# Optimization experiments

Hardware: AMD Instinct MI355X
Metric: run time of the kernel (lower is better)

The kernel has to match this reference:

```python
import jax, jax.numpy as jnp
import numpy as np

HID = 2048
H = 16
D_NOPE = 128
D_ROPE = 64
HEAD_DIM = D_NOPE + D_ROPE  # 192
V_DIM = 128
KV_RANK = 512
Q_RANK = 1536
THETA = 10000.0
EPS = 1e-6
B, S = 2, 2048


def _rope_cos_sin(seq_len):
    # half-dim frequencies: cos/sin have shape (seq_len, D_ROPE//2)
    inv_freq = 1.0 / (THETA ** (jnp.arange(0, D_ROPE, 2, dtype=jnp.float32) / D_ROPE))
    freqs = jnp.arange(seq_len, dtype=jnp.float32)[:, None] * inv_freq[None, :]
    return jnp.cos(freqs), jnp.sin(freqs)


def _apply_rope(x, cos, sin):
    # x: (..., D_ROPE); cos/sin broadcastable to (..., D_ROPE//2)
    half = x.shape[-1] // 2
    x1, x2 = x[..., :half], x[..., half:]
    return jnp.concatenate([x1 * cos - x2 * sin, x2 * cos + x1 * sin], axis=-1)


def _rmsnorm(x, w):
    ms = jnp.mean(jnp.square(x), axis=-1, keepdims=True)
    return x * jax.lax.rsqrt(ms + EPS) * w


def setup_inputs() -> dict:
    key = jax.random.key(0)
    ks = jax.random.split(key, 7)
    std = 0.02
    return {
        "x": jax.random.normal(ks[0], (B, S, HID), dtype=jnp.float32),
        "w_q_down": jax.random.normal(ks[1], (HID, Q_RANK), dtype=jnp.float32) * std,
        "w_q_up": jax.random.normal(ks[2], (Q_RANK, H * HEAD_DIM), dtype=jnp.float32) * std,
        "w_kv_down": jax.random.normal(ks[3], (HID, KV_RANK + D_ROPE), dtype=jnp.float32) * std,
        "kv_norm_w": jnp.ones((KV_RANK,), dtype=jnp.float32),
        "w_kv_up": jax.random.normal(ks[4], (KV_RANK, H * (D_NOPE + V_DIM)), dtype=jnp.float32) * std,
        "w_out": jax.random.normal(ks[5], (H * V_DIM, HID), dtype=jnp.float32) * std,
    }


def reference(x, w_q_down, w_q_up, w_kv_down, kv_norm_w, w_kv_up, w_out):
    b, s, _ = x.shape
    scale = 1.0 / np.sqrt(HEAD_DIM)

    # query: low-rank down then up, split into nope/rope parts
    q = (x @ w_q_down) @ w_q_up                      # (b, s, H*HEAD_DIM)
    q = q.reshape(b, s, H, HEAD_DIM)
    q_nope, q_rope = q[..., :D_NOPE], q[..., D_NOPE:]

    # KV: compressed latent + rope key component
    kv_full = x @ w_kv_down                          # (b, s, KV_RANK + D_ROPE)
    kv_c, k_rope = kv_full[..., :KV_RANK], kv_full[..., KV_RANK:]
    kv_c = _rmsnorm(kv_c, kv_norm_w)

    kv_exp = (kv_c @ w_kv_up).reshape(b, s, H, D_NOPE + V_DIM)
    k_nope, v = kv_exp[..., :D_NOPE], kv_exp[..., D_NOPE:]

    # RoPE (no past_kv -> q_offset = 0, kv_len = s)
    cos, sin = _rope_cos_sin(s)                      # (s, D_ROPE//2)
    cos4, sin4 = cos[None, :, None, :], sin[None, :, None, :]
    q_rope = _apply_rope(q_rope, cos4, sin4)         # (b, s, H, D_ROPE)
    k_rope = _apply_rope(k_rope, cos[None], sin[None])  # (b, s, D_ROPE)

    k_rope_h = jnp.broadcast_to(k_rope[:, :, None, :], (b, s, H, D_ROPE))
    k = jnp.concatenate([k_nope, k_rope_h], axis=-1)     # (b, s, H, HEAD_DIM)
    q_full = jnp.concatenate([q_nope, q_rope], axis=-1)  # (b, s, H, HEAD_DIM)

    # causal SDPA
    scores = jnp.einsum("bqhd,bkhd->bhqk", q_full, k) * scale
    causal = jnp.tril(jnp.ones((s, s), dtype=bool))
    scores = jnp.where(causal[None, None], scores, jnp.finfo(scores.dtype).min)
    attn = jax.nn.softmax(scores, axis=-1)
    out = jnp.einsum("bhqk,bkhd->bqhd", attn, v)     # (b, s, H, V_DIM)
    out = out.reshape(b, s, H * V_DIM)
    return out @ w_out
```

## Files before the change

kernel.cpp:

```cpp
#include <hip/hip_runtime.h>
#include <hip/hip_bf16.h>
#include <math.h>

#define HID    2048
#define NH     16
#define D_NOPE 128
#define D_ROPE 64
#define HD     192
#define V_DIM  128
#define KV_RANK 512
#define Q_RANK  1536
#define BATCH  2
#define SEQ    2048
#define ROWS   (BATCH*SEQ)

typedef __attribute__((ext_vector_type(8))) short short8;
typedef __attribute__((ext_vector_type(4))) float f32x4;

__device__ __forceinline__ unsigned short f2bf(float x) {
    unsigned int u = __float_as_uint(x);
    unsigned int r = (u + 0x7fffu + ((u >> 16) & 1u)) >> 16;
    return (unsigned short)r;
}
__device__ __forceinline__ float bf2f(unsigned short u) {
    return __uint_as_float((unsigned int)u << 16);
}

typedef const __attribute__((address_space(1))) unsigned int gu32;
typedef __attribute__((address_space(3))) unsigned int lu32;
__device__ __forceinline__ void gl_lds16(const void* g, void* l) {
    __builtin_amdgcn_global_load_lds((gu32*)g, (lu32*)l, 16, 0, 0);
}

template<int CTRL>
__device__ __forceinline__ float dpp_mv(float x) {
    return __int_as_float(__builtin_amdgcn_update_dpp(
        __float_as_int(x), __float_as_int(x), CTRL, 0xF, 0xF, true));
}
__device__ __forceinline__ float rowmax16(float x) {
    x = fmaxf(x, dpp_mv<0xB1>(x));
    x = fmaxf(x, dpp_mv<0x4E>(x));
    x = fmaxf(x, dpp_mv<0x141>(x));
    x = fmaxf(x, dpp_mv<0x140>(x));
    return x;
}

__global__ __launch_bounds__(256) void preprocess_kernel(
    const float* __restrict__ x,
    const float* __restrict__ w_q_down, const float* __restrict__ w_q_up,
    const float* __restrict__ w_kv_down, const float* __restrict__ w_kv_up,
    const float* __restrict__ w_out,
    float* __restrict__ table, unsigned short* __restrict__ xb,
    unsigned short* __restrict__ wt1, unsigned short* __restrict__ wt2,
    unsigned short* __restrict__ wt3, unsigned short* __restrict__ wt4,
    unsigned short* __restrict__ wt5)
{
    const int tid = threadIdx.x;
    int bid = blockIdx.x;

    if (bid < 512) {
        int idx = bid * 256 + tid;
        int pos = idx >> 6, u = idx & 63;
        int i = u & 31;
        float invf = expf((float)i * (-9.210340371976184f / 32.0f));
        float ang = (float)pos * invf;
        table[idx] = (u < 32) ? cosf(ang) : sinf(ang);
        return;
    }
    bid -= 512;
    if (bid < 8192) {
        size_t i = (size_t)(bid * 256 + tid) * 4;
        float4 v = *(const float4*)(x + i);
        ushort4 u;
        u.x = f2bf(v.x); u.y = f2bf(v.y); u.z = f2bf(v.z); u.w = f2bf(v.w);
        *(ushort4*)(xb + i) = u;
        return;
    }
    bid -= 8192;

    const float* src; unsigned short* dst; int K, N, gx, lb;
    if (bid < 768)       { src = w_q_down;  dst = wt1; K = 2048; N = 1536; gx = 24; lb = bid; }
    else if (bid < 1920) { src = w_q_up;    dst = wt2; K = 1536; N = 3072; gx = 48; lb = bid - 768; }
    else if (bid < 2208) { src = w_kv_down; dst = wt3; K = 2048; N = 576;  gx = 9;  lb = bid - 1920; }
    else if (bid < 2720) { src = w_kv_up;   dst = wt4; K = 512;  N = 4096; gx = 64; lb = bid - 2208; }
    else                 { src = w_out;     dst = wt5; K = 2048; N = 2048; gx = 32; lb = bid - 2720; }
    const int n0 = (lb % gx) * 64, k0 = (lb / gx) * 64;

    __shared__ float T[64][65];
    const int c4 = tid & 15, r = tid >> 4;
    #pragma unroll
    for (int i = 0; i < 4; i++) {
        int row = r + i * 16;
        float4 v = *(const float4*)(src + (size_t)(k0 + row) * N + n0 + c4 * 4);
        T[row][c4*4+0] = v.x; T[row][c4*4+1] = v.y;
        T[row][c4*4+2] = v.z; T[row][c4*4+3] = v.w;
    }
    __syncthreads();
    #pragma unroll
    for (int i = 0; i < 4; i++) {
        int nrow = r + i * 16;
        ushort4 u;
        u.x = f2bf(T[c4*4+0][nrow]); u.y = f2bf(T[c4*4+1][nrow]);
        u.z = f2bf(T[c4*4+2][nrow]); u.w = f2bf(T[c4*4+3][nrow]);
        *(ushort4*)(dst + (size_t)(n0 + nrow) * K + k0 + c4 * 4) = u;
    }
}

extern __shared__ unsigned short smem_gemm[];

template<int BN, bool OUT_BF16>
__device__ __forceinline__ void bgemm_body(
    int rbid, int nb,
    const unsigned short* __restrict__ A,
    const unsigned short* __restrict__ Bt,
    void* __restrict__ Cv,
    int M, int N, int K)
{
    constexpr int NT = BN / 32;
    constexpr int NSLAB = 8 + BN / 16;
    const int tid  = threadIdx.x;
    const int w    = tid >> 6;
    const int lane = tid & 63;
    const int n16  = lane & 15, quad = lane >> 4;

    const int T8   = nb >> 3;
    const int nbid = (rbid & 7) * T8 + (rbid >> 3);
    const int gx   = N / BN;
    const int m0 = (nbid / gx) * 128;
    const int n0 = (nbid % gx) * BN;
    const int moff = (w & 1) * 64;
    const int noff = (w >> 1) * (NT * 16);

    unsigned short* As = smem_gemm;
    unsigned short* Bs = smem_gemm + 128*32;

    const unsigned short* gp[4];
    unsigned short* lp[4];
    int ns = 0;
    const int rl = lane >> 2, sc = lane & 3;
    for (int s = w; s < NSLAB; s += 4) {
        int kc = sc ^ (((s * 16 + rl) >> 1) & 3);
        if (s < 8) {
            gp[ns] = A + (size_t)(m0 + s * 16 + rl) * K + kc * 8;
            lp[ns] = As + s * 512;
        } else {
            int sb = s - 8;
            gp[ns] = Bt + (size_t)(n0 + sb * 16 + rl) * K + kc * 8;
            lp[ns] = Bs + sb * 512;
        }
        ns++;
    }

    const int swz = (quad ^ ((n16 >> 1) & 3)) * 8;
    int aoff[4], boff[NT];
    #pragma unroll
    for (int mt = 0; mt < 4; mt++) aoff[mt] = (moff + mt * 16 + n16) * 32 + swz;
    #pragma unroll
    for (int nt = 0; nt < NT; nt++) boff[nt] = (noff + nt * 16 + n16) * 32 + swz;

    f32x4 acc[4][NT];
    #pragma unroll
    for (int mt = 0; mt < 4; mt++)
        #pragma unroll
        for (int nt = 0; nt < NT; nt++) acc[mt][nt] = (f32x4){0.f, 0.f, 0.f, 0.f};

    for (int k0 = 0; k0 < K; k0 += 32) {
        #pragma unroll
        for (int j = 0; j < 4; j++) if (j < ns) gl_lds16(gp[j], lp[j]);
        #pragma unroll
        for (int j = 0; j < 4; j++) if (j < ns) gp[j] += 32;
        __syncthreads();

        short8 af[4], bfr[NT];
        #pragma unroll
        for (int mt = 0; mt < 4; mt++) af[mt] = *(const short8*)(As + aoff[mt]);
        #pragma unroll
        for (int nt = 0; nt < NT; nt++) bfr[nt] = *(const short8*)(Bs + boff[nt]);
        #pragma unroll
        for (int mt = 0; mt < 4; mt++)
            #pragma unroll
            for (int nt = 0; nt < NT; nt++)
                acc[mt][nt] = __builtin_amdgcn_mfma_f32_16x16x32_bf16(
                    af[mt], bfr[nt], acc[mt][nt], 0, 0, 0);
        __syncthreads();
    }

    #pragma unroll
    for (int mt = 0; mt < 4; mt++)
        #pragma unroll
        for (int nt = 0; nt < NT; nt++)
            #pragma unroll
            for (int r = 0; r < 4; r++) {
                size_t idx = (size_t)(m0 + moff + mt * 16 + quad * 4 + r) * N
                           + n0 + noff + nt * 16 + n16;
                if (OUT_BF16) ((unsigned short*)Cv)[idx] = f2bf(acc[mt][nt][r]);
                else          ((float*)Cv)[idx] = acc[mt][nt][r];
            }
}

__global__ __launch_bounds__(256) void gemm_stage1_kernel(
    const unsigned short* __restrict__ xb,
    const unsigned short* __restrict__ wt1, const unsigned short* __restrict__ wt3,
    unsigned short* __restrict__ qdb, float* __restrict__ kv_full)
{
    if (blockIdx.x < 384)
        bgemm_body<128, true>(blockIdx.x, 384, xb, wt1, qdb, ROWS, 1536, 2048);
    else
        bgemm_body<64, false>(blockIdx.x - 384, 288, xb, wt3, kv_full, ROWS, 576, 2048);
}

__global__ __launch_bounds__(256) void gemm_stage2_kernel(
    const unsigned short* __restrict__ qdb, const unsigned short* __restrict__ wt2,
    const unsigned short* __restrict__ kv_cb, const unsigned short* __restrict__ wt4,
    unsigned short* __restrict__ qb16, unsigned short* __restrict__ kv_exp_b)
{
    if (blockIdx.x < 768)
        bgemm_body<128, true>(blockIdx.x, 768, qdb, wt2, qb16, ROWS, 3072, 1536);
    else
        bgemm_body<128, true>(blockIdx.x - 768, 1024, kv_cb, wt4, kv_exp_b, ROWS, 4096, 512);
}

__global__ __launch_bounds__(256) void gemm_out_kernel(
    const unsigned short* __restrict__ attnb, const unsigned short* __restrict__ wt5,
    float* __restrict__ out)
{
    bgemm_body<128, false>(blockIdx.x, 512, attnb, wt5, out, ROWS, 2048, 2048);
}

__global__ __launch_bounds__(256) void kv_norm_rope_kernel(
    const float* __restrict__ kv_full,
    const float* __restrict__ w,
    const float* __restrict__ table,
    unsigned short* __restrict__ kv_cb,
    unsigned short* __restrict__ k_rope_b)
{
    const int row = blockIdx.x;
    const int tid = threadIdx.x;
    const float* src = kv_full + (size_t)row * 576;
    float v0 = src[tid], v1 = src[tid + 256];
    float ss = v0*v0 + v1*v1;
    #pragma unroll
    for (int off = 32; off > 0; off >>= 1) ss += __shfl_down(ss, off);
    __shared__ float red[4];
    __shared__ float msh;
    if ((tid & 63) == 0) red[tid >> 6] = ss;
    __syncthreads();
    if (tid == 0) msh = (red[0] + red[1] + red[2] + red[3]) * (1.0f / 512.0f);
    __syncthreads();
    float f = rsqrtf(msh + 1e-6f);
    kv_cb[(size_t)row * 512 + tid]       = f2bf(v0 * f * w[tid]);
    kv_cb[(size_t)row * 512 + tid + 256] = f2bf(v1 * f * w[tid + 256]);
    if (tid < 32) {
        int pos = row & (SEQ - 1);
        float c = table[pos*64 + tid], s = table[pos*64 + 32 + tid];
        float x1 = src[512 + tid], x2 = src[512 + 32 + tid];
        k_rope_b[(size_t)row * 64 + tid]      = f2bf(x1*c - x2*s);
        k_rope_b[(size_t)row * 64 + 32 + tid] = f2bf(x2*c + x1*s);
    }
}

__global__ __launch_bounds__(256) void pack_vt_kernel(
    const unsigned short* __restrict__ kv_exp_b, unsigned short* __restrict__ Vmat)
{
    const int st = blockIdx.x;
    const int h  = blockIdx.y;
    const int b  = blockIdx.z;
    const int tid = threadIdx.x;
    const int s0 = st * 64;
    __shared__ float T[64][129];

    #pragma unroll
    for (int t = 0; t < 8; t++) {
        int idx = tid + t * 256;
        int tokr = idx >> 5, c4 = idx & 31;
        ushort4 u = *(const ushort4*)(kv_exp_b +
            ((size_t)(b*SEQ) + s0 + tokr) * 4096 + h*256 + 128 + c4*4);
        T[tokr][c4*4+0] = bf2f(u.x); T[tokr][c4*4+1] = bf2f(u.y);
        T[tokr][c4*4+2] = bf2f(u.z); T[tokr][c4*4+3] = bf2f(u.w);
    }
    __syncthreads();

    int d = tid >> 1, sh = (tid & 1) * 32;
    unsigned short* op = Vmat + ((size_t)((b*NH + h) * V_DIM + d)) * SEQ + s0 + sh;
    #pragma unroll
    for (int j = 0; j < 32; j += 2) {
        ushort2 u;
        u.x = f2bf(T[sh + j][d]);
        u.y = f2bf(T[sh + j + 1][d]);
        *(ushort2*)(op + j) = u;
    }
}

__global__ __launch_bounds__(256, 3) void flash_mfma_kernel(
    const unsigned short* __restrict__ qb16,
    const unsigned short* __restrict__ kv_exp_b,
    const unsigned short* __restrict__ k_rope_b,
    const unsigned short* __restrict__ Vmat,
    const float* __restrict__ table,
    unsigned short* __restrict__ attnb)
{
    const int bid  = blockIdx.x;
    const int xcd  = bid & 7, slot = bid >> 3;
    const int grp  = xcd + 8 * (slot >> 5);
    const int qb   = 31 - (slot & 31);
    const int h    = grp & 15, b = grp >> 4;
    const int tid  = threadIdx.x;
    const int w    = tid >> 6;
    const int lane = tid & 63;
    const int n16  = lane & 15;
    const int quad = lane >> 4;

    const int q0 = qb * 64 + w * 16;
    const char* kNopeB = (const char*)(kv_exp_b + (size_t)b * SEQ * 4096 + h * 256);
    const char* kRopeB = (const char*)(k_rope_b + (size_t)b * SEQ * 64);
    const char* vByte  = (const char*)(Vmat + (size_t)(b*NH + h) * V_DIM * SEQ);

    __shared__ unsigned short Ks[2][6144];
    __shared__ unsigned short Vs[2][4096];
    __shared__ unsigned short Plds[4][16][40];

    const char* gK[2]; int lK[2];
    #pragma unroll
    for (int t = 0; t < 2; t++) {
        int idx = t * 256 + tid;
        int kc = idx >> 7, key = (idx >> 2) & 31, sc = idx & 3;
        int scs = sc ^ ((key >> 1) & 3);
        gK[t] = kNopeB + (size_t)key * 8192 + kc * 64 + scs * 16;
        lK[t] = idx * 16;
    }
    const char* gR; int lR;
    {
        int kc = tid >> 7, key = (tid >> 2) & 31, sc = tid & 3;
        int scs = sc ^ ((key >> 1) & 3);
        gR = kRopeB + (size_t)key * 128 + kc * 64 + scs * 16;
        lR = (512 + tid) * 16;
    }
    const char* gV[2]; int lV[2];
    #pragma unroll
    for (int t = 0; t < 2; t++) {
        int idx = t * 256 + tid;
        int d = idx >> 2, sc = idx & 3;
        int scs = sc ^ ((d >> 1) & 3);
        gV[t] = vByte + (size_t)d * (SEQ * 2) + scs * 16;
        lV[t] = idx * 16;
    }

    auto stage = [&](int kt, int bufsel) {
        const size_t koff = (size_t)kt * 32;
        #pragma unroll
        for (int t = 0; t < 2; t++)
            gl_lds16(gK[t] + koff * 8192, (char*)Ks[bufsel] + lK[t]);
        gl_lds16(gR + koff * 128, (char*)Ks[bufsel] + lR);
        #pragma unroll
        for (int t = 0; t < 2; t++)
            gl_lds16(gV[t] + koff * 2, (char*)Vs[bufsel] + lV[t]);
    };

    short8 qf[6];
    {
        const unsigned short* qp = qb16 + ((size_t)(b*SEQ) + q0 + n16) * (NH*HD)
                                 + h * HD + quad * 8;
        #pragma unroll
        for (int kc = 0; kc < 6; kc++)
            qf[kc] = *(const short8*)(qp + kc * 32);
        const float* tb = table + (size_t)(q0 + n16) * 64 + quad * 8;
        float4 c0 = *(const float4*)(tb);
        float4 c1 = *(const float4*)(tb + 4);
        float4 s0 = *(const float4*)(tb + 32);
        float4 s1 = *(const float4*)(tb + 36);
        float cs[8] = {c0.x,c0.y,c0.z,c0.w,c1.x,c1.y,c1.z,c1.w};
        float sn[8] = {s0.x,s0.y,s0.z,s0.w,s1.x,s1.y,s1.z,s1.w};
        #pragma unroll
        for (int j = 0; j < 8; j++) {
            float x1 = bf2f((unsigned short)qf[4][j]);
            float x2 = bf2f((unsigned short)qf[5][j]);
            qf[4][j] = (short)f2bf(x1*cs[j] - x2*sn[j]);
            qf[5][j] = (short)f2bf(x2*cs[j] + x1*sn[j]);
        }
    }

    short8 onesf;
    #pragma unroll
    for (int j = 0; j < 8; j++) onesf[j] = (short)0x3F80;

    f32x4 O[9];
    #pragma unroll
    for (int c = 0; c < 9; c++) O[c] = (f32x4){0.f, 0.f, 0.f, 0.f};
    float mrow[4] = {-INFINITY, -INFINITY, -INFINITY, -INFINITY};

    const float SCLOG2 = 0.10412779736150104f;
    const float THRRAW = 83.14f;
    const int swz = (quad ^ ((n16 >> 1) & 3)) * 8;
    const int ntB = 2 * qb + 2;

    stage(0, 0);
    int cur = 0;
    for (int kt = 0; kt < ntB; kt++) {
        __syncthreads();
        if (kt + 1 < ntB) stage(kt + 1, cur ^ 1);
        const int k0 = kt * 32;

        if (k0 <= q0 + 15) {
            const unsigned short* KsB = Ks[cur];
            const unsigned short* VsB = Vs[cur];

            f32x4 S[2];
            __builtin_amdgcn_s_setprio(1);
            #pragma unroll
            for (int half = 0; half < 2; half++) {
                f32x4 acc = (f32x4){0.f, 0.f, 0.f, 0.f};
                const int keyoff = (half * 16 + n16) * 32 + swz;
                #pragma unroll
                for (int kc = 0; kc < 6; kc++) {
                    short8 kf = *(const short8*)(KsB + kc * 1024 + keyoff);
                    acc = __builtin_amdgcn_mfma_f32_16x16x32_bf16(qf[kc], kf, acc, 0, 0, 0);
                }
                S[half] = acc;
            }
            __builtin_amdgcn_s_setprio(0);

            float p0[4], p1[4];
            if (k0 + 32 > q0) {
                #pragma unroll
                for (int r = 0; r < 4; r++) {
                    int row = q0 + quad*4 + r;
                    p0[r] = (k0 + n16      <= row) ? S[0][r] : -INFINITY;
                    p1[r] = (k0 + 16 + n16 <= row) ? S[1][r] : -INFINITY;
                }
            } else {
                #pragma unroll
                for (int r = 0; r < 4; r++) { p0[r] = S[0][r]; p1[r] = S[1][r]; }
            }

            float tmax[4];
            float growth = -INFINITY;
            #pragma unroll
            for (int r = 0; r < 4; r++) {
                tmax[r] = rowmax16(fmaxf(p0[r], p1[r]));
                growth = fmaxf(growth, tmax[r] - mrow[r]);
            }
            if (!__all(growth <= THRRAW)) {
                #pragma unroll
                for (int r = 0; r < 4; r++) {
                    float mnew = fmaxf(mrow[r], tmax[r]);
                    float alpha = exp2f((mrow[r] - mnew) * SCLOG2);
                    mrow[r] = mnew;
                    #pragma unroll
                    for (int c = 0; c < 9; c++) O[c][r] *= alpha;
                }
            }
            #pragma unroll
            for (int r = 0; r < 4; r++) {
                float e0 = exp2f((p0[r] - mrow[r]) * SCLOG2);
                float e1 = exp2f((p1[r] - mrow[r]) * SCLOG2);
                unsigned int pk;
                asm("v_cvt_pk_bf16_f32 %0, %1, %2" : "=v"(pk) : "v"(e0), "v"(e1));
                unsigned short* pw = &Plds[w][quad*4 + r][0];
                pw[n16]      = (unsigned short)(pk & 0xffffu);
                pw[16 + n16] = (unsigned short)(pk >> 16);
            }

            short8 pf = *(const short8*)(&Plds[w][n16][quad * 8]);
            __builtin_amdgcn_s_setprio(1);
            #pragma unroll
            for (int c = 0; c < 8; c++) {
                short8 vf = *(const short8*)(VsB + (c * 16 + n16) * 32 + swz);
                O[c] = __builtin_amdgcn_mfma_f32_16x16x32_bf16(pf, vf, O[c], 0, 0, 0);
            }
            O[8] = __builtin_amdgcn_mfma_f32_16x16x32_bf16(pf, onesf, O[8], 0, 0, 0);
            __builtin_amdgcn_s_setprio(0);
        }
        cur ^= 1;
    }

    float invl[4];
    #pragma unroll
    for (int r = 0; r < 4; r++) invl[r] = 1.0f / O[8][r];
    #pragma unroll
    for (int c = 0; c < 8; c++) {
        #pragma unroll
        for (int r = 0; r < 4; r++) {
            size_t tok = (size_t)b * SEQ + q0 + quad*4 + r;
            attnb[tok * (NH*V_DIM) + h * V_DIM + c*16 + n16] = f2bf(O[c][r] * invl[r]);
        }
    }
}

extern "C" void kernel_launch(void* const* d_in, const int* in_sizes, int n_in,
                              void* d_out, int out_size, void* d_ws, size_t ws_size,
                              hipStream_t stream)
{
    const float* x         = (const float*)d_in[0];
    const float* w_q_down  = (const float*)d_in[1];
    const float* w_q_up    = (const float*)d_in[2];
    const float* w_kv_down = (const float*)d_in[3];
    const float* kv_norm_w = (const float*)d_in[4];
    const float* w_kv_up   = (const float*)d_in[5];
    const float* w_out     = (const float*)d_in[6];
    float* out = (float*)d_out;
    float* ws  = (float*)d_ws;

    float*          table    = ws;
    unsigned short* xb       = (unsigned short*)(ws + 131072);
    unsigned short* qdb      = (unsigned short*)(ws + 4325376);
    unsigned short* qb16     = (unsigned short*)(ws + 7471104);
    float*          kv_full  = ws + 13762560;
    unsigned short* kv_cb    = (unsigned short*)(ws + 16121856);
    unsigned short* k_rope_b = (unsigned short*)(ws + 17170432);
    unsigned short* kv_exp_b = (unsigned short*)(ws + 17301504);
    unsigned short* Vmat     = (unsigned short*)(ws + 25690112);
    unsigned short* attnb    = (unsigned short*)(ws + 29884416);
    unsigned short* wt1      = (unsigned short*)(ws + 34078720);
    unsigned short* wt2      = (unsigned short*)(ws + 35651584);
    unsigned short* wt3      = (unsigned short*)(ws + 38010880);
    unsigned short* wt4      = (unsigned short*)(ws + 38600704);
    unsigned short* wt5      = (unsigned short*)(ws + 39649280);

    preprocess_kernel<<<dim3(12448), 256, 0, stream>>>(
        x, w_q_down, w_q_up, w_kv_down, w_kv_up, w_out,
        table, xb, wt1, wt2, wt3, wt4, wt5);

    gemm_stage1_kernel<<<dim3(672), 256, 16384, stream>>>(xb, wt1, wt3, qdb, kv_full);

    kv_norm_rope_kernel<<<ROWS, 256, 0, stream>>>(kv_full, kv_norm_w, table, kv_cb, k_rope_b);

    gemm_stage2_kernel<<<dim3(1792), 256, 16384, stream>>>(qdb, wt2, kv_cb, wt4, qb16, kv_exp_b);

    pack_vt_kernel<<<dim3(SEQ/64, NH, BATCH), 256, 0, stream>>>(kv_exp_b, Vmat);

    flash_mfma_kernel<<<dim3(1024), 256, 0, stream>>>(qb16, kv_exp_b, k_rope_b, Vmat, table, attnb);

    gemm_out_kernel<<<dim3(512), 256, 16384, stream>>>(attnb, wt5, out);
}
```

Before: 431.3 us.

## Fuse V transpose into kv-up GEMM epilogue and shrink GEMM M-tiles

The kv-up GEMM epilogue now writes V tiles straight into the transposed Vmat layout with 4-token vector stores, so the separate pack_vt kernel and its extra read of kv_exp_b go away. The GEMM template also gains a BM parameter, and stage1 and the output GEMM switch to 64-row tiles with twice the blocks, aimed at better CU occupancy and load balance. Smaller tiles mean less reuse of each B tile. The transposed epilogue stores are strided by SEQ, which may coalesce worse.

```diff
diff --git a/kernel.cpp b/kernel.cpp
--- a/kernel.cpp
+++ b/kernel.cpp
@@ -108,16 +108,18 @@
 
 extern __shared__ unsigned short smem_gemm[];
 
-template<int BN, bool OUT_BF16>
+template<int BM, int BN, bool OUT_BF16, bool VSTORE>
 __device__ __forceinline__ void bgemm_body(
     int rbid, int nb,
     const unsigned short* __restrict__ A,
     const unsigned short* __restrict__ Bt,
     void* __restrict__ Cv,
+    unsigned short* __restrict__ vmat,
     int M, int N, int K)
 {
+    constexpr int MT = BM / 32;
     constexpr int NT = BN / 32;
-    constexpr int NSLAB = 8 + BN / 16;
+    constexpr int NSLAB = BM / 16 + BN / 16;
     const int tid  = threadIdx.x;
     const int w    = tid >> 6;
     const int lane = tid & 63;
@@ -126,13 +128,13 @@
     const int T8   = nb >> 3;
     const int nbid = (rbid & 7) * T8 + (rbid >> 3);
     const int gx   = N / BN;
-    const int m0 = (nbid / gx) * 128;
+    const int m0 = (nbid / gx) * BM;
     const int n0 = (nbid % gx) * BN;
-    const int moff = (w & 1) * 64;
+    const int moff = (w & 1) * (MT * 16);
     const int noff = (w >> 1) * (NT * 16);
 
     unsigned short* As = smem_gemm;
-    unsigned short* Bs = smem_gemm + 128*32;
+    unsigned short* Bs = smem_gemm + BM*32;
 
     const unsigned short* gp[4];
     unsigned short* lp[4];
@@ -140,11 +142,11 @@
     const int rl = lane >> 2, sc = lane & 3;
     for (int s = w; s < NSLAB; s += 4) {
         int kc = sc ^ (((s * 16 + rl) >> 1) & 3);
-        if (s < 8) {
+        if (s < BM/16) {
             gp[ns] = A + (size_t)(m0 + s * 16 + rl) * K + kc * 8;
             lp[ns] = As + s * 512;
         } else {
-            int sb = s - 8;
+            int sb = s - BM/16;
             gp[ns] = Bt + (size_t)(n0 + sb * 16 + rl) * K + kc * 8;
             lp[ns] = Bs + sb * 512;
         }
@@ -152,15 +154,15 @@
     }
 
     const int swz = (quad ^ ((n16 >> 1) & 3)) * 8;
-    int aoff[4], boff[NT];
-    #pragma unroll
-    for (int mt = 0; mt < 4; mt++) aoff[mt] = (moff + mt * 16 + n16) * 32 + swz;
+    int aoff[MT], boff[NT];
+    #pragma unroll
+    for (int mt = 0; mt < MT; mt++) aoff[mt] = (moff + mt * 16 + n16) * 32 + swz;
     #pragma unroll
     for (int nt = 0; nt < NT; nt++) boff[nt] = (noff + nt * 16 + n16) * 32 + swz;
 
-    f32x4 acc[4][NT];
-    #pragma unroll
-    for (int mt = 0; mt < 4; mt++)
+    f32x4 acc[MT][NT];
+    #pragma unroll
+    for (int mt = 0; mt < MT; mt++)
         #pragma unroll
         for (int nt = 0; nt < NT; nt++) acc[mt][nt] = (f32x4){0.f, 0.f, 0.f, 0.f};
 
@@ -171,13 +173,13 @@
         for (int j = 0; j < 4; j++) if (j < ns) gp[j] += 32;
         __syncthreads();
 
-        short8 af[4], bfr[NT];
-        #pragma unroll
-        for (int mt = 0; mt < 4; mt++) af[mt] = *(const short8*)(As + aoff[mt]);
+        short8 af[MT], bfr[NT];
+        #pragma unroll
+        for (int mt = 0; mt < MT; mt++) af[mt] = *(const short8*)(As + aoff[mt]);
         #pragma unroll
         for (int nt = 0; nt < NT; nt++) bfr[nt] = *(const short8*)(Bs + boff[nt]);
         #pragma unroll
-        for (int mt = 0; mt < 4; mt++)
+        for (int mt = 0; mt < MT; mt++)
             #pragma unroll
             for (int nt = 0; nt < NT; nt++)
                 acc[mt][nt] = __builtin_amdgcn_mfma_f32_16x16x32_bf16(
@@ -185,8 +187,27 @@
         __syncthreads();
     }
 
-    #pragma unroll
-    for (int mt = 0; mt < 4; mt++)
+    if (VSTORE && ((n0 >> 7) & 1)) {
+        const int hh = n0 >> 8;
+        #pragma unroll
+        for (int mt = 0; mt < MT; mt++) {
+            int token = m0 + moff + mt * 16 + quad * 4;
+            int bb = token >> 11, ti = token & (SEQ - 1);
+            unsigned short* vb = vmat + (size_t)(bb*NH + hh) * V_DIM * SEQ + ti;
+            #pragma unroll
+            for (int nt = 0; nt < NT; nt++) {
+                int d = noff + nt * 16 + n16;
+                ushort4 u;
+                u.x = f2bf(acc[mt][nt][0]); u.y = f2bf(acc[mt][nt][1]);
+                u.z = f2bf(acc[mt][nt][2]); u.w = f2bf(acc[mt][nt][3]);
+                *(ushort4*)(vb + (size_t)d * SEQ) = u;
+            }
+        }
+        return;
+    }
+
+    #pragma unroll
+    for (int mt = 0; mt < MT; mt++)
         #pragma unroll
         for (int nt = 0; nt < NT; nt++)
             #pragma unroll
@@ -203,28 +224,29 @@
     const unsigned short* __restrict__ wt1, const unsigned short* __restrict__ wt3,
     unsigned short* __restrict__ qdb, float* __restrict__ kv_full)
 {
-    if (blockIdx.x < 384)
-        bgemm_body<128, true>(blockIdx.x, 384, xb, wt1, qdb, ROWS, 1536, 2048);
+    if (blockIdx.x < 768)
+        bgemm_body<64, 128, true, false>(blockIdx.x, 768, xb, wt1, qdb, nullptr, ROWS, 1536, 2048);
     else
-        bgemm_body<64, false>(blockIdx.x - 384, 288, xb, wt3, kv_full, ROWS, 576, 2048);
+        bgemm_body<64, 64, false, false>(blockIdx.x - 768, 576, xb, wt3, kv_full, nullptr, ROWS, 576, 2048);
 }
 
 __global__ __launch_bounds__(256) void gemm_stage2_kernel(
     const unsigned short* __restrict__ qdb, const unsigned short* __restrict__ wt2,
     const unsigned short* __restrict__ kv_cb, const unsigned short* __restrict__ wt4,
-    unsigned short* __restrict__ qb16, unsigned short* __restrict__ kv_exp_b)
+    unsigned short* __restrict__ qb16, unsigned short* __restrict__ kv_exp_b,
+    unsigned short* __restrict__ Vmat)
 {
     if (blockIdx.x < 768)
-        bgemm_body<128, true>(blockIdx.x, 768, qdb, wt2, qb16, ROWS, 3072, 1536);
+        bgemm_body<128, 128, true, false>(blockIdx.x, 768, qdb, wt2, qb16, nullptr, ROWS, 3072, 1536);
     else
-        bgemm_body<128, true>(blockIdx.x - 768, 1024, kv_cb, wt4, kv_exp_b, ROWS, 4096, 512);
+        bgemm_body<128, 128, true, true>(blockIdx.x - 768, 1024, kv_cb, wt4, kv_exp_b, Vmat, ROWS, 4096, 512);
 }
 
 __global__ __launch_bounds__(256) void gemm_out_kernel(
     const unsigned short* __restrict__ attnb, const unsigned short* __restrict__ wt5,
     float* __restrict__ out)
 {
-    bgemm_body<128, false>(blockIdx.x, 512, attnb, wt5, out, ROWS, 2048, 2048);
+    bgemm_body<64, 128, false, false>(blockIdx.x, 1024, attnb, wt5, out, nullptr, ROWS, 2048, 2048);
 }
 
 __global__ __launch_bounds__(256) void kv_norm_rope_kernel(
@@ -259,38 +281,6 @@
     }
 }
 
-__global__ __launch_bounds__(256) void pack_vt_kernel(
-    const unsigned short* __restrict__ kv_exp_b, unsigned short* __restrict__ Vmat)
-{
-    const int st = blockIdx.x;
-    const int h  = blockIdx.y;
-    const int b  = blockIdx.z;
-    const int tid = threadIdx.x;
-    const int s0 = st * 64;
-    __shared__ float T[64][129];
-
-    #pragma unroll
-    for (int t = 0; t < 8; t++) {
-        int idx = tid + t * 256;
-        int tokr = idx >> 5, c4 = idx & 31;
-        ushort4 u = *(const ushort4*)(kv_exp_b +
-            ((size_t)(b*SEQ) + s0 + tokr) * 4096 + h*256 + 128 + c4*4);
-        T[tokr][c4*4+0] = bf2f(u.x); T[tokr][c4*4+1] = bf2f(u.y);
-        T[tokr][c4*4+2] = bf2f(u.z); T[tokr][c4*4+3] = bf2f(u.w);
-    }
-    __syncthreads();
-
-    int d = tid >> 1, sh = (tid & 1) * 32;
-    unsigned short* op = Vmat + ((size_t)((b*NH + h) * V_DIM + d)) * SEQ + s0 + sh;
-    #pragma unroll
-    for (int j = 0; j < 32; j += 2) {
-        ushort2 u;
-        u.x = f2bf(T[sh + j][d]);
-        u.y = f2bf(T[sh + j + 1][d]);
-        *(ushort2*)(op + j) = u;
-    }
-}
-
 __global__ __launch_bounds__(256, 3) void flash_mfma_kernel(
     const unsigned short* __restrict__ qb16,
     const unsigned short* __restrict__ kv_exp_b,
@@ -520,15 +510,13 @@
         x, w_q_down, w_q_up, w_kv_down, w_kv_up, w_out,
         table, xb, wt1, wt2, wt3, wt4, wt5);
 
-    gemm_stage1_kernel<<<dim3(672), 256, 16384, stream>>>(xb, wt1, wt3, qdb, kv_full);
+    gemm_stage1_kernel<<<dim3(1344), 256, 16384, stream>>>(xb, wt1, wt3, qdb, kv_full);
 
     kv_norm_rope_kernel<<<ROWS, 256, 0, stream>>>(kv_full, kv_norm_w, table, kv_cb, k_rope_b);
 
-    gemm_stage2_kernel<<<dim3(1792), 256, 16384, stream>>>(qdb, wt2, kv_cb, wt4, qb16, kv_exp_b);
-
-    pack_vt_kernel<<<dim3(SEQ/64, NH, BATCH), 256, 0, stream>>>(kv_exp_b, Vmat);
+    gemm_stage2_kernel<<<dim3(1792), 256, 16384, stream>>>(qdb, wt2, kv_cb, wt4, qb16, kv_exp_b, Vmat);
 
     flash_mfma_kernel<<<dim3(1024), 256, 0, stream>>>(qb16, kv_exp_b, k_rope_b, Vmat, table, attnb);
 
-    gemm_out_kernel<<<dim3(512), 256, 16384, stream>>>(attnb, wt5, out);
-}
+    gemm_out_kernel<<<dim3(1024), 256, 16384, stream>>>(attnb, wt5, out);
+}
```

Result: slower. 467.7 us (+8.4%).
